# Kernel tuning notes

Measured on AMD Instinct MI355X. Metric: run time of the kernel, lower is better.

## Reference

```python
import jax, jax.numpy as jnp
import numpy as np

H = 6            # nheads
DPH = 200.0      # dim_per_head buffer = mha_dimension / nheads (used as divisor, NOT sqrt)
EPS = 1e-5


def layernorm(x, g, b):
    m = jnp.mean(x, axis=-1, keepdims=True)
    v = jnp.mean((x - m) ** 2, axis=-1, keepdims=True)
    return (x - m) * jax.lax.rsqrt(v + EPS) * g + b


def leaky(x):
    # torch.nn.LeakyReLU(True) -> negative_slope = 1.0 (identity), kept for faithfulness
    return jnp.where(x >= 0, x, 1.0 * x)


def setup_inputs() -> dict:
    key = jax.random.key(0)
    ks = jax.random.split(key, 16)
    B, L, D, M = 4, 2048, 512, 1200
    s_in = 1.0 / np.sqrt(D)
    s_m = 1.0 / np.sqrt(M)
    return {
        "query": jax.random.normal(ks[0], (B, L, D), jnp.float32),
        "keyval": jax.random.normal(ks[1], (B, 1, D), jnp.float32),
        "Wq": jax.random.normal(ks[2], (D, M), jnp.float32) * s_in,
        "bq": jnp.zeros((M,), jnp.float32),
        "Wkv": jax.random.normal(ks[3], (D, 2 * M), jnp.float32) * s_in,
        "bkv": jnp.zeros((2 * M,), jnp.float32),
        "Wff": jax.random.normal(ks[4], (M, D), jnp.float32) * s_m,
        "bff": jnp.zeros((D,), jnp.float32),
        "g1": jnp.ones((D,), jnp.float32),
        "b1": jnp.zeros((D,), jnp.float32),
        "W2a": jax.random.normal(ks[5], (D, 4 * D), jnp.float32) * s_in,
        "b2a": jnp.zeros((4 * D,), jnp.float32),
        "W2b": jax.random.normal(ks[6], (4 * D, D), jnp.float32) / np.sqrt(4 * D),
        "b2b": jnp.zeros((D,), jnp.float32),
        "g2": jnp.ones((D,), jnp.float32),
        "b2": jnp.zeros((D,), jnp.float32),
    }


def reference(query, keyval, Wq, bq, Wkv, bkv, Wff, bff, g1, b1,
              W2a, b2a, W2b, b2b, g2, b2):
    B, L, D = query.shape
    kv = jnp.broadcast_to(keyval, query.shape)           # keyval.expand_as(query)
    Q = query @ Wq + bq                                  # [B,L,M]
    KV = kv @ Wkv + bkv                                  # [B,L,2M]
    K, V = jnp.split(KV, 2, axis=-1)

    def heads(x):  # b l (h d) -> b h l d
        return x.reshape(B, L, H, -1).transpose(0, 2, 1, 3)

    Qh, Kh, Vh = heads(Q), heads(K), heads(V)
    logits = jnp.einsum('bhid,bhjd->bhij', Qh, Kh) / DPH  # note: / d, not / sqrt(d)
    sm = jax.nn.softmax(logits, axis=-1)                  # [B,H,L,L]
    mha = jnp.einsum('bhij,bhjd->bhid', sm, Vh)
    mha_ = mha.transpose(0, 2, 1, 3).reshape(B, L, -1)    # b h i d -> b i (h d)

    out = mha_ @ Wff + bff                                # dropout = identity (eval)
    out_ = layernorm(out + query, g1, b1)
    out2 = leaky(out_ @ W2a + b2a) @ W2b + b2b
    out3 = layernorm(out_ + out2, g2, b2)
    out3 = out3 + kv
    return out3, sm
```

## Files before the change

### kernel.cpp

```cpp
#include <hip/hip_runtime.h>
#include <hip/hip_bf16.h>


typedef __bf16 bf16x8 __attribute__((ext_vector_type(8)));
typedef float f32x4 __attribute__((ext_vector_type(4)));

constexpr size_t OUT3_N = 4ull * 2048 * 512;
constexpr size_t SM_N4  = (4ull * 6 * 2048 * 2048) / 4;
constexpr float  SMV    = 1.0f / 2048.0f;

constexpr size_t S1 = 0,        C1 = 5375000;
constexpr size_t S3 = 5375000,  C3 = 5687500;
constexpr size_t S4 = 11062500, C4 = 4750000;
constexpr size_t S5 = 15812500, C5 = 5187500;
constexpr size_t S6 = 21000000, C6 = 4165824;
static_assert(S6 + C6 == SM_N4, "fill slices must cover sm");

__device__ __forceinline__ void fill_slice(f32x4* __restrict__ p, size_t base, size_t cnt,
                                           int fb, int nfb){
    const f32x4 v = { SMV, SMV, SMV, SMV };
    const size_t stride = (size_t)nfb * 256;
    for (size_t j = (size_t)fb * 256 + threadIdx.x; j < cnt; j += stride)
        __builtin_nontemporal_store(v, p + base + j);
}

template<int MODE, typename OutT>
__device__ void gemm_tile(const __bf16* __restrict__ A, const __bf16* __restrict__ BT,
                          OutT* __restrict__ C, int Ndim, int Kdim,
                          int bm, int bn, int k0beg, int k0end){
    __shared__ __bf16 As[64 * 64];
    __shared__ __bf16 Bs[64 * 64];
    const int tid = threadIdx.x, wave = tid >> 6, lane = tid & 63;
    const int r_st = wave * 8 + (lane >> 3);
    const int c8g  = (lane & 7) ^ (r_st & 7);
    const __bf16* Ag = A  + (size_t)(bm + r_st) * Kdim + c8g * 8;
    const __bf16* Bg = BT + (size_t)(bn + r_st) * Kdim + c8g * 8;
    const size_t rowskip = (size_t)32 * Kdim;
    const int wm = (wave >> 1) * 32, wn = (wave & 1) * 32;
    const int lm = lane & 15, lq = lane >> 4;
    f32x4 acc[2][2] = {};
    for (int k0 = k0beg; k0 < k0end; k0 += 64){
        __builtin_amdgcn_global_load_lds(
            (const __attribute__((address_space(1))) void*)(Ag + k0),
            (__attribute__((address_space(3))) void*)&As[wave * 512], 16, 0, 0);
        __builtin_amdgcn_global_load_lds(
            (const __attribute__((address_space(1))) void*)(Ag + k0 + rowskip),
            (__attribute__((address_space(3))) void*)&As[2048 + wave * 512], 16, 0, 0);
        __builtin_amdgcn_global_load_lds(
            (const __attribute__((address_space(1))) void*)(Bg + k0),
            (__attribute__((address_space(3))) void*)&Bs[wave * 512], 16, 0, 0);
        __builtin_amdgcn_global_load_lds(
            (const __attribute__((address_space(1))) void*)(Bg + k0 + rowskip),
            (__attribute__((address_space(3))) void*)&Bs[2048 + wave * 512], 16, 0, 0);
        __syncthreads();
        #pragma unroll
        for (int kb = 0; kb < 64; kb += 32){
            const int sw = (((kb >> 3) + lq) ^ (lm & 7)) << 3;
            bf16x8 a0 = *(const bf16x8*)&As[(wm + lm) * 64 + sw];
            bf16x8 a1 = *(const bf16x8*)&As[(wm + 16 + lm) * 64 + sw];
            bf16x8 b0 = *(const bf16x8*)&Bs[(wn + lm) * 64 + sw];
            bf16x8 b1 = *(const bf16x8*)&Bs[(wn + 16 + lm) * 64 + sw];
            acc[0][0] = __builtin_amdgcn_mfma_f32_16x16x32_bf16(a0, b0, acc[0][0], 0, 0, 0);
            acc[0][1] = __builtin_amdgcn_mfma_f32_16x16x32_bf16(a0, b1, acc[0][1], 0, 0, 0);
            acc[1][0] = __builtin_amdgcn_mfma_f32_16x16x32_bf16(a1, b0, acc[1][0], 0, 0, 0);
            acc[1][1] = __builtin_amdgcn_mfma_f32_16x16x32_bf16(a1, b1, acc[1][1], 0, 0, 0);
        }
        __syncthreads();
    }
    #pragma unroll
    for (int mi = 0; mi < 2; ++mi)
      #pragma unroll
      for (int ni = 0; ni < 2; ++ni)
        #pragma unroll
        for (int r = 0; r < 4; ++r){
            int row = bm + wm + mi * 16 + lq * 4 + r;
            int col = bn + wn + ni * 16 + lm;
            if (MODE == 1) atomicAdd((float*)&C[(size_t)row * Ndim + col], acc[mi][ni][r]);
            else           C[(size_t)row * Ndim + col] = (OutT)acc[mi][ni][r];
        }
}

__global__ __launch_bounds__(256) void k1_prep_kv(const float* __restrict__ W2a,
        const float* __restrict__ b2a, __bf16* __restrict__ A1,
        const float* __restrict__ W2b, __bf16* __restrict__ W2bT,
        const float* __restrict__ keyval, const float* __restrict__ Wkv,
        const float* __restrict__ bkv, float* __restrict__ V, f32x4* __restrict__ smf){
    __shared__ float sh[32 * 33];
    const int bid = blockIdx.x, tid = threadIdx.x;
    if (bid < 1152){
        int r = bid >> 1;
        int c = (bid & 1) * 1024 + tid * 4;
        float4 v;
        if (r < 512)       v = *(const float4*)(W2a + (size_t)r * 2048 + c);
        else if (r == 512) v = *(const float4*)(b2a + c);
        else               v = make_float4(0.f, 0.f, 0.f, 0.f);
        __bf16* o = A1 + (size_t)r * 2048 + c;
        o[0] = (__bf16)v.x; o[1] = (__bf16)v.y; o[2] = (__bf16)v.z; o[3] = (__bf16)v.w;
    } else if (bid < 2176){
        int t = bid - 1152;
        int c0 = (t & 15) * 32, r0 = (t >> 4) * 32;
        int tx = tid & 31, ty = tid >> 5;
        for (int i = ty; i < 32; i += 8)
            sh[i * 33 + tx] = W2b[(size_t)(r0 + i) * 512 + c0 + tx];
        __syncthreads();
        for (int i = ty; i < 32; i += 8)
            W2bT[(size_t)(c0 + i) * 2048 + r0 + tx] = (__bf16)sh[tx * 33 + i];
    } else if (bid < 2336){
        int i = bid - 2176;
        int b = i & 3, mc = (i >> 2) % 5, kc = i / 20;
        int m = mc * 256 + tid;
        if (m < 1200){
            float acc = (kc == 0) ? bkv[1200 + m] : 0.f;
            const float* kvb = keyval + (size_t)b * 512;
            int d0 = kc * 64;
            #pragma unroll 8
            for (int d = d0; d < d0 + 64; ++d)
                acc += kvb[d] * Wkv[(size_t)d * 2400 + 1200 + m];
            atomicAdd(&V[b * 1200 + m], acc);
        }
    }
    fill_slice(smf, S1, C1, bid, 2848);
}

__global__ __launch_bounds__(256) void k3_fold_oc(const __bf16* __restrict__ A1,
        const __bf16* __restrict__ W2bT, float* __restrict__ Wf,
        const float* __restrict__ V, const float* __restrict__ Wff,
        const float* __restrict__ bff, float* __restrict__ oc, f32x4* __restrict__ smf){
    const int bid = blockIdx.x, tid = threadIdx.x;
    if (bid < 288){
        int tile = bid % 72, kc = bid / 72;
        gemm_tile<1>(A1, W2bT, Wf, 512, 2048, (tile % 9) * 64, (tile / 9) * 64,
                     kc * 512, (kc + 1) * 512);
    } else if (bid < 384){
        int i = bid - 288;
        int b = i & 3, jc = (i >> 2) & 1, kc = i >> 3;
        int j = jc * 256 + tid;
        float acc = (kc == 0) ? bff[j] : 0.f;
        const float* vb = V + b * 1200;
        int m0 = kc * 100;
        #pragma unroll 5
        for (int m = m0; m < m0 + 100; ++m)
            acc += vb[m] * Wff[(size_t)m * 512 + j];
        atomicAdd(&oc[b * 512 + j], acc);
    }
    fill_slice(smf, S3, C3, bid, 2048);
}

__global__ __launch_bounds__(256) void k4_ln1_tcast(const float* __restrict__ q,
        const float* __restrict__ oc, const float* __restrict__ g1,
        const float* __restrict__ b1, __bf16* __restrict__ Xb,
        const float* __restrict__ Wf, __bf16* __restrict__ WfT, f32x4* __restrict__ smf){
    __shared__ float sh[32 * 33];
    const int bid = blockIdx.x, t = threadIdx.x;
    if (bid < 8192){
        const int b = bid >> 11;
        const size_t base = (size_t)bid * 512;
        float2 qv = *(const float2*)(q + base + 2 * t);
        float2 ov = *(const float2*)(oc + (size_t)b * 512 + 2 * t);
        float v0 = qv.x + ov.x, v1 = qv.y + ov.y;
        float s = v0 + v1, ss = v0 * v0 + v1 * v1;
        for (int off = 32; off; off >>= 1){ s += __shfl_down(s, off); ss += __shfl_down(ss, off); }
        int wv = t >> 6, ln = t & 63;
        if (ln == 0){ sh[wv] = s; sh[4 + wv] = ss; }
        __syncthreads();
        if (t == 0){
            float S  = sh[0] + sh[1] + sh[2] + sh[3];
            float SS = sh[4] + sh[5] + sh[6] + sh[7];
            float m = S * (1.0f / 512.0f);
            float var = SS * (1.0f / 512.0f) - m * m;
            sh[0] = m; sh[1] = rsqrtf(var + 1e-5f);
        }
        __syncthreads();
        float m = sh[0], r = sh[1];
        float2 gv = *(const float2*)(g1 + 2 * t);
        float2 bv = *(const float2*)(b1 + 2 * t);
        union { __bf16 h[2]; unsigned u; } pk;
        pk.h[0] = (__bf16)((v0 - m) * r * gv.x + bv.x);
        pk.h[1] = (__bf16)((v1 - m) * r * gv.y + bv.y);
        *(unsigned*)(Xb + base + 2 * t) = pk.u;
    } else if (bid < 8448){
        int tt = bid - 8192;
        int c0 = (tt & 15) * 32, r0 = (tt >> 4) * 32;
        int tx = t & 31, ty = t >> 5;
        for (int i = ty; i < 32; i += 8)
            sh[i * 33 + tx] = Wf[(size_t)(r0 + i) * 512 + c0 + tx];
        __syncthreads();
        for (int i = ty; i < 32; i += 8)
            WfT[(size_t)(c0 + i) * 512 + r0 + tx] = (__bf16)sh[tx * 33 + i];
    }
    fill_slice(smf, S4, C4, bid, 8960);
}

__global__ __launch_bounds__(256) void k5_gemm(const __bf16* __restrict__ X,
        const __bf16* __restrict__ WfT, __bf16* __restrict__ out2, f32x4* __restrict__ smf){
    const int bid = blockIdx.x;
    if (bid < 1024){
        gemm_tile<2>(X, WfT, out2, 512, 512, (bid >> 3) * 64, (bid & 7) * 64, 0, 512);
    }
    fill_slice(smf, S5, C5, bid, 2048);
}

__global__ __launch_bounds__(256) void k6_ln2(const __bf16* __restrict__ X,
        const __bf16* __restrict__ o2, const float* __restrict__ bfrow,
        const float* __restrict__ b2b, const float* __restrict__ g2,
        const float* __restrict__ b2, const float* __restrict__ keyval,
        float* __restrict__ out3, f32x4* __restrict__ smf){
    __shared__ float sh[8];
    const int bid = blockIdx.x, t = threadIdx.x;
    if (bid < 8192){
        const int b = bid >> 11;
        const size_t base = (size_t)bid * 512;
        union { unsigned u; __bf16 h[2]; } xv, yv;
        xv.u = *(const unsigned*)(X + base + 2 * t);
        yv.u = *(const unsigned*)(o2 + base + 2 * t);
        float f0 = bfrow[2 * t] + b2b[2 * t], f1 = bfrow[2 * t + 1] + b2b[2 * t + 1];
        float v0 = (float)xv.h[0] + (float)yv.h[0] + f0;
        float v1 = (float)xv.h[1] + (float)yv.h[1] + f1;
        float s = v0 + v1, ss = v0 * v0 + v1 * v1;
        for (int off = 32; off; off >>= 1){ s += __shfl_down(s, off); ss += __shfl_down(ss, off); }
        int wv = t >> 6, ln = t & 63;
        if (ln == 0){ sh[wv] = s; sh[4 + wv] = ss; }
        __syncthreads();
        if (t == 0){
            float S  = sh[0] + sh[1] + sh[2] + sh[3];
            float SS = sh[4] + sh[5] + sh[6] + sh[7];
            float m = S * (1.0f / 512.0f);
            float var = SS * (1.0f / 512.0f) - m * m;
            sh[0] = m; sh[1] = rsqrtf(var + 1e-5f);
        }
        __syncthreads();
        float m = sh[0], r = sh[1];
        float2 gv = *(const float2*)(g2 + 2 * t);
        float2 bv = *(const float2*)(b2 + 2 * t);
        float2 kv = *(const float2*)(keyval + (size_t)b * 512 + 2 * t);
        float y0 = (v0 - m) * r * gv.x + bv.x + kv.x;
        float y1 = (v1 - m) * r * gv.y + bv.y + kv.y;
        *(float2*)(out3 + base + 2 * t) = make_float2(y0, y1);
    }
    fill_slice(smf, S6, C6, bid, 8704);
}

extern "C" void kernel_launch(void* const* d_in, const int* in_sizes, int n_in,
                              void* d_out, int out_size, void* d_ws, size_t ws_size,
                              hipStream_t stream){
    const float* query  = (const float*)d_in[0];
    const float* keyval = (const float*)d_in[1];
    const float* Wkv = (const float*)d_in[4];
    const float* bkv = (const float*)d_in[5];
    const float* Wff = (const float*)d_in[6];
    const float* bff = (const float*)d_in[7];
    const float* g1  = (const float*)d_in[8];
    const float* b1  = (const float*)d_in[9];
    const float* W2a = (const float*)d_in[10];
    const float* b2a = (const float*)d_in[11];
    const float* W2b = (const float*)d_in[12];
    const float* b2b = (const float*)d_in[13];
    const float* g2  = (const float*)d_in[14];
    const float* b2  = (const float*)d_in[15];

    float* out3 = (float*)d_out;
    f32x4* smf  = (f32x4*)(out3 + OUT3_N);

    char* base = (ws_size >= (64ull << 20)) ? (char*)d_ws : (char*)smf;
    float*  t_Wf   = (float*)base;
    float*  t_V    = t_Wf + 294912;
    float*  t_oc   = t_V + 4800;
    __bf16* t_A1   = (__bf16*)(t_oc + 2048);
    __bf16* t_W2bT = t_A1 + 1179648;
    __bf16* t_WfT  = t_W2bT + 1048576;
    __bf16* t_X    = t_WfT + 262144;
    __bf16* t_out2 = t_X + 4194304;

    (void)hipMemsetAsync(t_Wf, 0, 301760 * sizeof(float), stream);
    k1_prep_kv<<<2848, 256, 0, stream>>>(W2a, b2a, t_A1, W2b, t_W2bT,
                                         keyval, Wkv, bkv, t_V, smf);
    k3_fold_oc<<<2048, 256, 0, stream>>>(t_A1, t_W2bT, t_Wf, t_V, Wff, bff, t_oc, smf);
    k4_ln1_tcast<<<8960, 256, 0, stream>>>(query, t_oc, g1, b1, t_X, t_Wf, t_WfT, smf);
    k5_gemm<<<2048, 256, 0, stream>>>(t_X, t_WfT, t_out2, smf);
    k6_ln2<<<8704, 256, 0, stream>>>(t_X, t_out2, t_Wf + 262144, b2b, g2, b2,
                                     keyval, out3, smf);
}
```

Measured before the change: 488.0 us.

## Fuse FFN GEMM with LayerNorm2 and drop split-K atomics and memset

The second GEMM and LayerNorm2 become one kernel. Each block computes a full 16x512 output row tile, so the LayerNorm statistics are reduced in registers and shared memory, and the bf16 intermediate out2 is no longer written to and read back from memory. The folded weight GEMM now runs without split-K and writes the transposed bf16 WfT and the bias row directly, which removes the atomics, the memset and the separate transpose pass. The V and oc reductions also drop atomics. The cost is that the fold GEMM now uses only 72 blocks and the fused kernel holds a large 64KB B tile in shared memory, which reduces parallelism and occupancy.

```diff
diff --git a/kernel.cpp b/kernel.cpp
--- a/kernel.cpp
+++ b/kernel.cpp
@@ -9,12 +9,11 @@
 constexpr size_t SM_N4  = (4ull * 6 * 2048 * 2048) / 4;
 constexpr float  SMV    = 1.0f / 2048.0f;
 
-constexpr size_t S1 = 0,        C1 = 5375000;
-constexpr size_t S3 = 5375000,  C3 = 5687500;
-constexpr size_t S4 = 11062500, C4 = 4750000;
-constexpr size_t S5 = 15812500, C5 = 5187500;
-constexpr size_t S6 = 21000000, C6 = 4165824;
-static_assert(S6 + C6 == SM_N4, "fill slices must cover sm");
+constexpr size_t S1  = 0,        C1  = 7000000;
+constexpr size_t S3  = 7000000,  C3  = 6900000;
+constexpr size_t S4  = 13900000, C4  = 6500000;
+constexpr size_t S56 = 20400000, C56 = 4765824;
+static_assert(S56 + C56 == SM_N4, "fill slices must cover sm");
 
 __device__ __forceinline__ void fill_slice(f32x4* __restrict__ p, size_t base, size_t cnt,
                                            int fb, int nfb){
@@ -24,22 +23,21 @@
         __builtin_nontemporal_store(v, p + base + j);
 }
 
-template<int MODE, typename OutT>
-__device__ void gemm_tile(const __bf16* __restrict__ A, const __bf16* __restrict__ BT,
-                          OutT* __restrict__ C, int Ndim, int Kdim,
-                          int bm, int bn, int k0beg, int k0end){
+__device__ void gemm_wf(const __bf16* __restrict__ A, const __bf16* __restrict__ BT,
+                        __bf16* __restrict__ WfT, float* __restrict__ fb,
+                        const float* __restrict__ b2b, int bm, int bn){
     __shared__ __bf16 As[64 * 64];
     __shared__ __bf16 Bs[64 * 64];
     const int tid = threadIdx.x, wave = tid >> 6, lane = tid & 63;
     const int r_st = wave * 8 + (lane >> 3);
     const int c8g  = (lane & 7) ^ (r_st & 7);
-    const __bf16* Ag = A  + (size_t)(bm + r_st) * Kdim + c8g * 8;
-    const __bf16* Bg = BT + (size_t)(bn + r_st) * Kdim + c8g * 8;
-    const size_t rowskip = (size_t)32 * Kdim;
+    const __bf16* Ag = A  + (size_t)(bm + r_st) * 2048 + c8g * 8;
+    const __bf16* Bg = BT + (size_t)(bn + r_st) * 2048 + c8g * 8;
+    const size_t rowskip = (size_t)32 * 2048;
     const int wm = (wave >> 1) * 32, wn = (wave & 1) * 32;
     const int lm = lane & 15, lq = lane >> 4;
     f32x4 acc[2][2] = {};
-    for (int k0 = k0beg; k0 < k0end; k0 += 64){
+    for (int k0 = 0; k0 < 2048; k0 += 64){
         __builtin_amdgcn_global_load_lds(
             (const __attribute__((address_space(1))) void*)(Ag + k0),
             (__attribute__((address_space(3))) void*)&As[wave * 512], 16, 0, 0);
@@ -75,12 +73,12 @@
         for (int r = 0; r < 4; ++r){
             int row = bm + wm + mi * 16 + lq * 4 + r;
             int col = bn + wn + ni * 16 + lm;
-            if (MODE == 1) atomicAdd((float*)&C[(size_t)row * Ndim + col], acc[mi][ni][r]);
-            else           C[(size_t)row * Ndim + col] = (OutT)acc[mi][ni][r];
-        }
-}
-
-__global__ __launch_bounds__(256) void k1_prep_kv(const float* __restrict__ W2a,
+            if (row < 512)       WfT[(size_t)col * 512 + row] = (__bf16)acc[mi][ni][r];
+            else if (row == 512) fb[col] = acc[mi][ni][r] + b2b[col];
+        }
+}
+
+__global__ __launch_bounds__(256) void k1_prep(const float* __restrict__ W2a,
         const float* __restrict__ b2a, __bf16* __restrict__ A1,
         const float* __restrict__ W2b, __bf16* __restrict__ W2bT,
         const float* __restrict__ keyval, const float* __restrict__ Wkv,
@@ -105,52 +103,54 @@
         __syncthreads();
         for (int i = ty; i < 32; i += 8)
             W2bT[(size_t)(c0 + i) * 2048 + r0 + tx] = (__bf16)sh[tx * 33 + i];
-    } else if (bid < 2336){
+    } else if (bid < 2196){
         int i = bid - 2176;
-        int b = i & 3, mc = (i >> 2) % 5, kc = i / 20;
-        int m = mc * 256 + tid;
-        if (m < 1200){
-            float acc = (kc == 0) ? bkv[1200 + m] : 0.f;
+        int b = i & 3, mc = i >> 2;
+        int m = mc * 240 + tid;
+        if (tid < 240){
+            float acc = bkv[1200 + m];
             const float* kvb = keyval + (size_t)b * 512;
-            int d0 = kc * 64;
             #pragma unroll 8
-            for (int d = d0; d < d0 + 64; ++d)
+            for (int d = 0; d < 512; ++d)
                 acc += kvb[d] * Wkv[(size_t)d * 2400 + 1200 + m];
-            atomicAdd(&V[b * 1200 + m], acc);
+            V[b * 1200 + m] = acc;
         }
     }
     fill_slice(smf, S1, C1, bid, 2848);
 }
 
-__global__ __launch_bounds__(256) void k3_fold_oc(const __bf16* __restrict__ A1,
-        const __bf16* __restrict__ W2bT, float* __restrict__ Wf,
+__global__ __launch_bounds__(256) void k3_wf_oc(const __bf16* __restrict__ A1,
+        const __bf16* __restrict__ W2bT, __bf16* __restrict__ WfT,
+        float* __restrict__ fb, const float* __restrict__ b2b,
         const float* __restrict__ V, const float* __restrict__ Wff,
         const float* __restrict__ bff, float* __restrict__ oc, f32x4* __restrict__ smf){
-    const int bid = blockIdx.x, tid = threadIdx.x;
-    if (bid < 288){
-        int tile = bid % 72, kc = bid / 72;
-        gemm_tile<1>(A1, W2bT, Wf, 512, 2048, (tile % 9) * 64, (tile / 9) * 64,
-                     kc * 512, (kc + 1) * 512);
-    } else if (bid < 384){
-        int i = bid - 288;
-        int b = i & 3, jc = (i >> 2) & 1, kc = i >> 3;
-        int j = jc * 256 + tid;
-        float acc = (kc == 0) ? bff[j] : 0.f;
+    const int bid = blockIdx.x, t = threadIdx.x;
+    if (bid < 72){
+        gemm_wf(A1, W2bT, WfT, fb, b2b, (bid % 9) * 64, (bid / 9) * 64);
+    } else if (bid < 104){
+        __shared__ float sh[4 * 64];
+        int i = bid - 72;
+        int b = i & 3, jc = i >> 2;
+        int wv = t >> 6, j = jc * 64 + (t & 63);
         const float* vb = V + b * 1200;
-        int m0 = kc * 100;
-        #pragma unroll 5
-        for (int m = m0; m < m0 + 100; ++m)
+        float acc = 0.f;
+        int m0 = wv * 300;
+        #pragma unroll 4
+        for (int m = m0; m < m0 + 300; ++m)
             acc += vb[m] * Wff[(size_t)m * 512 + j];
-        atomicAdd(&oc[b * 512 + j], acc);
+        sh[t] = acc;
+        __syncthreads();
+        if (t < 64)
+            oc[b * 512 + jc * 64 + t] = sh[t] + sh[64 + t] + sh[128 + t] + sh[192 + t]
+                                      + bff[jc * 64 + t];
     }
     fill_slice(smf, S3, C3, bid, 2048);
 }
 
-__global__ __launch_bounds__(256) void k4_ln1_tcast(const float* __restrict__ q,
+__global__ __launch_bounds__(256) void k4_ln1(const float* __restrict__ q,
         const float* __restrict__ oc, const float* __restrict__ g1,
-        const float* __restrict__ b1, __bf16* __restrict__ Xb,
-        const float* __restrict__ Wf, __bf16* __restrict__ WfT, f32x4* __restrict__ smf){
-    __shared__ float sh[32 * 33];
+        const float* __restrict__ b1, __bf16* __restrict__ Xb, f32x4* __restrict__ smf){
+    __shared__ float sh[8];
     const int bid = blockIdx.x, t = threadIdx.x;
     if (bid < 8192){
         const int b = bid >> 11;
@@ -178,66 +178,119 @@
         pk.h[0] = (__bf16)((v0 - m) * r * gv.x + bv.x);
         pk.h[1] = (__bf16)((v1 - m) * r * gv.y + bv.y);
         *(unsigned*)(Xb + base + 2 * t) = pk.u;
-    } else if (bid < 8448){
-        int tt = bid - 8192;
-        int c0 = (tt & 15) * 32, r0 = (tt >> 4) * 32;
-        int tx = t & 31, ty = t >> 5;
-        for (int i = ty; i < 32; i += 8)
-            sh[i * 33 + tx] = Wf[(size_t)(r0 + i) * 512 + c0 + tx];
-        __syncthreads();
-        for (int i = ty; i < 32; i += 8)
-            WfT[(size_t)(c0 + i) * 512 + r0 + tx] = (__bf16)sh[tx * 33 + i];
-    }
-    fill_slice(smf, S4, C4, bid, 8960);
-}
-
-__global__ __launch_bounds__(256) void k5_gemm(const __bf16* __restrict__ X,
-        const __bf16* __restrict__ WfT, __bf16* __restrict__ out2, f32x4* __restrict__ smf){
-    const int bid = blockIdx.x;
-    if (bid < 1024){
-        gemm_tile<2>(X, WfT, out2, 512, 512, (bid >> 3) * 64, (bid & 7) * 64, 0, 512);
-    }
-    fill_slice(smf, S5, C5, bid, 2048);
-}
-
-__global__ __launch_bounds__(256) void k6_ln2(const __bf16* __restrict__ X,
-        const __bf16* __restrict__ o2, const float* __restrict__ bfrow,
-        const float* __restrict__ b2b, const float* __restrict__ g2,
-        const float* __restrict__ b2, const float* __restrict__ keyval,
-        float* __restrict__ out3, f32x4* __restrict__ smf){
-    __shared__ float sh[8];
-    const int bid = blockIdx.x, t = threadIdx.x;
-    if (bid < 8192){
-        const int b = bid >> 11;
-        const size_t base = (size_t)bid * 512;
-        union { unsigned u; __bf16 h[2]; } xv, yv;
-        xv.u = *(const unsigned*)(X + base + 2 * t);
-        yv.u = *(const unsigned*)(o2 + base + 2 * t);
-        float f0 = bfrow[2 * t] + b2b[2 * t], f1 = bfrow[2 * t + 1] + b2b[2 * t + 1];
-        float v0 = (float)xv.h[0] + (float)yv.h[0] + f0;
-        float v1 = (float)xv.h[1] + (float)yv.h[1] + f1;
-        float s = v0 + v1, ss = v0 * v0 + v1 * v1;
-        for (int off = 32; off; off >>= 1){ s += __shfl_down(s, off); ss += __shfl_down(ss, off); }
-        int wv = t >> 6, ln = t & 63;
-        if (ln == 0){ sh[wv] = s; sh[4 + wv] = ss; }
-        __syncthreads();
-        if (t == 0){
-            float S  = sh[0] + sh[1] + sh[2] + sh[3];
-            float SS = sh[4] + sh[5] + sh[6] + sh[7];
+    }
+    fill_slice(smf, S4, C4, bid, 8704);
+}
+
+__global__ __launch_bounds__(256) void k56_gemm_ln2(const __bf16* __restrict__ X,
+        const __bf16* __restrict__ WfT, const float* __restrict__ fb,
+        const float* __restrict__ g2, const float* __restrict__ b2,
+        const float* __restrict__ keyval, float* __restrict__ out3,
+        f32x4* __restrict__ smf){
+    __shared__ __bf16 As[16 * 64];
+    __shared__ __bf16 Bs[512 * 64];
+    __shared__ float red[4 * 32];
+    __shared__ float stats[32];
+    const int bid = blockIdx.x, tid = threadIdx.x;
+    if (bid < 512){
+        const int wv = tid >> 6, lane = tid & 63;
+        const int lm = lane & 15, lq = lane >> 4;
+        const int r0 = bid * 16;
+        const int srow = lane >> 3;
+        const int c8 = lane & 7;
+        f32x4 acc[8] = {};
+        for (int k0 = 0; k0 < 512; k0 += 64){
+            if (wv == 0){
+                #pragma unroll
+                for (int i = 0; i < 2; ++i){
+                    int row = i * 8 + srow;
+                    const __bf16* src = X + (size_t)(r0 + row) * 512 + k0
+                                          + ((c8 ^ (row & 7)) << 3);
+                    __builtin_amdgcn_global_load_lds(
+                        (const __attribute__((address_space(1))) void*)src,
+                        (__attribute__((address_space(3))) void*)&As[i * 512], 16, 0, 0);
+                }
+            }
+            #pragma unroll
+            for (int i = 0; i < 16; ++i){
+                int nrow = wv * 128 + i * 8 + srow;
+                const __bf16* src = WfT + (size_t)nrow * 512 + k0
+                                        + ((c8 ^ (srow & 7)) << 3);
+                __builtin_amdgcn_global_load_lds(
+                    (const __attribute__((address_space(1))) void*)src,
+                    (__attribute__((address_space(3))) void*)&Bs[(wv * 128 + i * 8) * 64],
+                    16, 0, 0);
+            }
+            __syncthreads();
+            #pragma unroll
+            for (int kb = 0; kb < 64; kb += 32){
+                const int sw = (((kb >> 3) + lq) ^ (lm & 7)) << 3;
+                bf16x8 a = *(const bf16x8*)&As[lm * 64 + sw];
+                #pragma unroll
+                for (int ni = 0; ni < 8; ++ni){
+                    int n = wv * 128 + ni * 16 + lm;
+                    bf16x8 b = *(const bf16x8*)&Bs[n * 64 + sw];
+                    acc[ni] = __builtin_amdgcn_mfma_f32_16x16x32_bf16(a, b, acc[ni], 0, 0, 0);
+                }
+            }
+            __syncthreads();
+        }
+        const int b = bid >> 7;
+        float sum[4] = {}, ssum[4] = {};
+        #pragma unroll
+        for (int ni = 0; ni < 8; ++ni){
+            int col = wv * 128 + ni * 16 + lm;
+            float f = fb[col];
+            #pragma unroll
+            for (int jr = 0; jr < 4; ++jr){
+                int row = lq * 4 + jr;
+                float xv = (float)X[(size_t)(r0 + row) * 512 + col];
+                float val = acc[ni][jr] + xv + f;
+                acc[ni][jr] = val;
+                sum[jr] += val; ssum[jr] += val * val;
+            }
+        }
+        #pragma unroll
+        for (int msk = 1; msk < 16; msk <<= 1){
+            #pragma unroll
+            for (int jr = 0; jr < 4; ++jr){
+                sum[jr]  += __shfl_xor(sum[jr],  msk);
+                ssum[jr] += __shfl_xor(ssum[jr], msk);
+            }
+        }
+        if (lm == 0){
+            #pragma unroll
+            for (int jr = 0; jr < 4; ++jr){
+                red[wv * 32 + (lq * 4 + jr) * 2]     = sum[jr];
+                red[wv * 32 + (lq * 4 + jr) * 2 + 1] = ssum[jr];
+            }
+        }
+        __syncthreads();
+        if (tid < 16){
+            float S  = red[tid * 2]     + red[32 + tid * 2]
+                     + red[64 + tid * 2] + red[96 + tid * 2];
+            float SS = red[tid * 2 + 1] + red[32 + tid * 2 + 1]
+                     + red[64 + tid * 2 + 1] + red[96 + tid * 2 + 1];
             float m = S * (1.0f / 512.0f);
             float var = SS * (1.0f / 512.0f) - m * m;
-            sh[0] = m; sh[1] = rsqrtf(var + 1e-5f);
-        }
-        __syncthreads();
-        float m = sh[0], r = sh[1];
-        float2 gv = *(const float2*)(g2 + 2 * t);
-        float2 bv = *(const float2*)(b2 + 2 * t);
-        float2 kv = *(const float2*)(keyval + (size_t)b * 512 + 2 * t);
-        float y0 = (v0 - m) * r * gv.x + bv.x + kv.x;
-        float y1 = (v1 - m) * r * gv.y + bv.y + kv.y;
-        *(float2*)(out3 + base + 2 * t) = make_float2(y0, y1);
-    }
-    fill_slice(smf, S6, C6, bid, 8704);
+            stats[tid * 2] = m;
+            stats[tid * 2 + 1] = rsqrtf(var + 1e-5f);
+        }
+        __syncthreads();
+        #pragma unroll
+        for (int jr = 0; jr < 4; ++jr){
+            int row = lq * 4 + jr;
+            float m = stats[row * 2], ri = stats[row * 2 + 1];
+            #pragma unroll
+            for (int ni = 0; ni < 8; ++ni){
+                int col = wv * 128 + ni * 16 + lm;
+                float y = (acc[ni][jr] - m) * ri * g2[col] + b2[col]
+                        + keyval[(size_t)b * 512 + col];
+                out3[(size_t)(r0 + row) * 512 + col] = y;
+            }
+        }
+    }
+    fill_slice(smf, S56, C56, bid, 2048);
 }
 
 extern "C" void kernel_launch(void* const* d_in, const int* in_sizes, int n_in,
@@ -262,21 +315,19 @@
     f32x4* smf  = (f32x4*)(out3 + OUT3_N);
 
     char* base = (ws_size >= (64ull << 20)) ? (char*)d_ws : (char*)smf;
-    float*  t_Wf   = (float*)base;
-    float*  t_V    = t_Wf + 294912;
-    float*  t_oc   = t_V + 4800;
-    __bf16* t_A1   = (__bf16*)(t_oc + 2048);
+    __bf16* t_A1   = (__bf16*)base;
     __bf16* t_W2bT = t_A1 + 1179648;
     __bf16* t_WfT  = t_W2bT + 1048576;
     __bf16* t_X    = t_WfT + 262144;
-    __bf16* t_out2 = t_X + 4194304;
-
-    (void)hipMemsetAsync(t_Wf, 0, 301760 * sizeof(float), stream);
-    k1_prep_kv<<<2848, 256, 0, stream>>>(W2a, b2a, t_A1, W2b, t_W2bT,
-                                         keyval, Wkv, bkv, t_V, smf);
-    k3_fold_oc<<<2048, 256, 0, stream>>>(t_A1, t_W2bT, t_Wf, t_V, Wff, bff, t_oc, smf);
-    k4_ln1_tcast<<<8960, 256, 0, stream>>>(query, t_oc, g1, b1, t_X, t_Wf, t_WfT, smf);
-    k5_gemm<<<2048, 256, 0, stream>>>(t_X, t_WfT, t_out2, smf);
-    k6_ln2<<<8704, 256, 0, stream>>>(t_X, t_out2, t_Wf + 262144, b2b, g2, b2,
-                                     keyval, out3, smf);
-}
+    float*  t_V    = (float*)(t_X + 4194304);
+    float*  t_oc   = t_V + 4800;
+    float*  t_fb   = t_oc + 2048;
+
+    k1_prep<<<2848, 256, 0, stream>>>(W2a, b2a, t_A1, W2b, t_W2bT,
+                                      keyval, Wkv, bkv, t_V, smf);
+    k3_wf_oc<<<2048, 256, 0, stream>>>(t_A1, t_W2bT, t_WfT, t_fb, b2b,
+                                       t_V, Wff, bff, t_oc, smf);
+    k4_ln1<<<8704, 256, 0, stream>>>(query, t_oc, g1, b1, t_X, smf);
+    k56_gemm_ln2<<<2048, 256, 0, stream>>>(t_X, t_WfT, t_fb, g2, b2,
+                                           keyval, out3, smf);
+}
```

New measurement: 539.2 us. +10.5%, slower.

## Rewrite k5 GEMM with 64x128 tiles, direct global-to-LDS loads, and swizzled LDS

Applied to the files above, without the earlier changes.

The k5 GEMM (8192x512x512) now uses a dedicated 64x128 tile per block instead of the generic 64x64 gemm_tile helper. This halves the GEMM block count and loads tiles with global_load_lds into XOR-swizzled shared memory, aiming to cut register staging and LDS bank conflicts. It also packs the bf16 conversion stores in k1 into single 8-byte stores. The grid stays at 2048 blocks because the softmax fill dominates, so fewer blocks do GEMM work and the load may be less even across them.

```diff
diff --git a/kernel.cpp b/kernel.cpp
--- a/kernel.cpp
+++ b/kernel.cpp
@@ -94,8 +94,10 @@
         if (r < 512)       v = *(const float4*)(W2a + (size_t)r * 2048 + c);
         else if (r == 512) v = *(const float4*)(b2a + c);
         else               v = make_float4(0.f, 0.f, 0.f, 0.f);
-        __bf16* o = A1 + (size_t)r * 2048 + c;
-        o[0] = (__bf16)v.x; o[1] = (__bf16)v.y; o[2] = (__bf16)v.z; o[3] = (__bf16)v.w;
+        union { __bf16 h[4]; ushort4 u; } pk;
+        pk.h[0] = (__bf16)v.x; pk.h[1] = (__bf16)v.y;
+        pk.h[2] = (__bf16)v.z; pk.h[3] = (__bf16)v.w;
+        *(ushort4*)(A1 + (size_t)r * 2048 + c) = pk.u;
     } else if (bid < 2176){
         int t = bid - 1152;
         int c0 = (t & 15) * 32, r0 = (t >> 4) * 32;
@@ -194,8 +196,63 @@
 __global__ __launch_bounds__(256) void k5_gemm(const __bf16* __restrict__ X,
         const __bf16* __restrict__ WfT, __bf16* __restrict__ out2, f32x4* __restrict__ smf){
     const int bid = blockIdx.x;
-    if (bid < 1024){
-        gemm_tile<2>(X, WfT, out2, 512, 512, (bid >> 3) * 64, (bid & 7) * 64, 0, 512);
+    if (bid < 512){
+        __shared__ __bf16 As[64 * 64];
+        __shared__ __bf16 Bs[128 * 64];
+        const int bm = (bid >> 2) * 64, bn = (bid & 3) * 128;
+        const int tid = threadIdx.x, wave = tid >> 6, lane = tid & 63;
+        const int r_st = wave * 8 + (lane >> 3);
+        const int c8g  = (lane & 7) ^ (r_st & 7);
+        const __bf16* Ag = X   + (size_t)(bm + r_st) * 512 + c8g * 8;
+        const __bf16* Bg = WfT + (size_t)(bn + r_st) * 512 + c8g * 8;
+        const size_t rowskip = (size_t)32 * 512;
+        const int wm = (wave >> 1) * 32, wn = (wave & 1) * 64;
+        const int lm = lane & 15, lq = lane >> 4;
+        f32x4 acc[2][4] = {};
+        for (int k0 = 0; k0 < 512; k0 += 64){
+            __builtin_amdgcn_global_load_lds(
+                (const __attribute__((address_space(1))) void*)(Ag + k0),
+                (__attribute__((address_space(3))) void*)&As[wave * 512], 16, 0, 0);
+            __builtin_amdgcn_global_load_lds(
+                (const __attribute__((address_space(1))) void*)(Ag + k0 + rowskip),
+                (__attribute__((address_space(3))) void*)&As[2048 + wave * 512], 16, 0, 0);
+            #pragma unroll
+            for (int i = 0; i < 4; ++i)
+                __builtin_amdgcn_global_load_lds(
+                    (const __attribute__((address_space(1))) void*)(Bg + k0 + i * rowskip),
+                    (__attribute__((address_space(3))) void*)&Bs[i * 2048 + wave * 512],
+                    16, 0, 0);
+            __syncthreads();
+            #pragma unroll
+            for (int kb = 0; kb < 64; kb += 32){
+                const int sw = (((kb >> 3) + lq) ^ (lm & 7)) << 3;
+                bf16x8 a0 = *(const bf16x8*)&As[(wm + lm) * 64 + sw];
+                bf16x8 a1 = *(const bf16x8*)&As[(wm + 16 + lm) * 64 + sw];
+                bf16x8 b0 = *(const bf16x8*)&Bs[(wn + lm) * 64 + sw];
+                bf16x8 b1 = *(const bf16x8*)&Bs[(wn + 16 + lm) * 64 + sw];
+                bf16x8 b2 = *(const bf16x8*)&Bs[(wn + 32 + lm) * 64 + sw];
+                bf16x8 b3 = *(const bf16x8*)&Bs[(wn + 48 + lm) * 64 + sw];
+                acc[0][0] = __builtin_amdgcn_mfma_f32_16x16x32_bf16(a0, b0, acc[0][0], 0, 0, 0);
+                acc[0][1] = __builtin_amdgcn_mfma_f32_16x16x32_bf16(a0, b1, acc[0][1], 0, 0, 0);
+                acc[0][2] = __builtin_amdgcn_mfma_f32_16x16x32_bf16(a0, b2, acc[0][2], 0, 0, 0);
+                acc[0][3] = __builtin_amdgcn_mfma_f32_16x16x32_bf16(a0, b3, acc[0][3], 0, 0, 0);
+                acc[1][0] = __builtin_amdgcn_mfma_f32_16x16x32_bf16(a1, b0, acc[1][0], 0, 0, 0);
+                acc[1][1] = __builtin_amdgcn_mfma_f32_16x16x32_bf16(a1, b1, acc[1][1], 0, 0, 0);
+                acc[1][2] = __builtin_amdgcn_mfma_f32_16x16x32_bf16(a1, b2, acc[1][2], 0, 0, 0);
+                acc[1][3] = __builtin_amdgcn_mfma_f32_16x16x32_bf16(a1, b3, acc[1][3], 0, 0, 0);
+            }
+            __syncthreads();
+        }
+        #pragma unroll
+        for (int mi = 0; mi < 2; ++mi)
+          #pragma unroll
+          for (int ni = 0; ni < 4; ++ni)
+            #pragma unroll
+            for (int r = 0; r < 4; ++r){
+                int row = bm + wm + mi * 16 + lq * 4 + r;
+                int col = bn + wn + ni * 16 + lm;
+                out2[(size_t)row * 512 + col] = (__bf16)acc[mi][ni][r];
+            }
     }
     fill_slice(smf, S5, C5, bid, 2048);
 }
```

Result: no change. 485.2 us (-0.6%).
